# Kernel tuning notes

Hardware: AMD Instinct MI355X
Metric: run time of the kernel (lower is better)

The kernel has to match this reference:

```python
import jax, jax.numpy as jnp
import numpy as np

BS, GRID, LSTM_H, CNN_C, PROJ = 256, 49, 512, 2048, 512


def setup_inputs() -> dict:
    key = jax.random.key(0)
    ks = jax.random.split(key, 7)
    s = lambda fan_in: 1.0 / np.sqrt(fan_in)
    return {
        "lstm_hidden": jax.random.normal(ks[0], (BS, LSTM_H), jnp.float32),
        "cnn_feat": jax.random.normal(ks[1], (BS, GRID, CNN_C), jnp.float32),
        "W_lstm": jax.random.normal(ks[2], (PROJ, LSTM_H), jnp.float32) * s(LSTM_H),
        "b_lstm": jax.random.normal(ks[3], (PROJ,), jnp.float32) * s(LSTM_H),
        "W_cnn": jax.random.normal(ks[4], (PROJ, CNN_C), jnp.float32) * s(CNN_C),
        "b_cnn": jax.random.normal(ks[5], (PROJ,), jnp.float32) * s(CNN_C),
        "w_attn": jax.random.normal(ks[6], (1, PROJ), jnp.float32) * s(PROJ),
    }


def reference(lstm_hidden, cnn_feat, W_lstm, b_lstm, W_cnn, b_cnn, w_attn):
    # H computed once (original loop recomputes it per grid, identically)
    H = lstm_hidden @ W_lstm.T + b_lstm                       # (bs, P)
    V = jnp.einsum("bgc,pc->bgp", cnn_feat, W_cnn) + b_cnn    # (bs, G, P)
    z = jnp.tanh(H[:, None, :] + V) @ w_attn[0]               # (bs, G)
    bs, G = z.shape
    # Faithful to torch: cat over grids along dim 0 -> (G*bs,), then view(bs, G)
    z_scrambled = jnp.swapaxes(z, 0, 1).reshape(bs, G)
    return jax.nn.softmax(z_scrambled, axis=1)
```

## Files before the change

kernel.cpp:

```cpp
#include <hip/hip_runtime.h>
#include <math.h>

#define BSZ    256
#define GRID_N 49
#define LSTMH  512
#define CNN_C  2048
#define PROJ   512
#define KAUG   2560
#define M_TOT  12544
#define BK     64
#define KTILES (KAUG / BK)

#define MT2    128
#define NT2    128
#define NBLK2  ((M_TOT / MT2) * (PROJ / NT2))

#define MT     64
#define NT     128
#define NBLK   ((M_TOT / MT) * (PROJ / NT))

#define WBLK   640

typedef short bf16x8 __attribute__((ext_vector_type(8)));
typedef float f32x4  __attribute__((ext_vector_type(4)));

static __device__ __forceinline__ unsigned short bf16_rne(float f) {
    unsigned int u = __float_as_uint(f);
    u = u + 0x7FFFu + ((u >> 16) & 1u);
    return (unsigned short)(u >> 16);
}
static __device__ __forceinline__ uint4 pack8f(const float* f) {
    uint4 o;
    o.x = (unsigned int)bf16_rne(f[0]) | ((unsigned int)bf16_rne(f[1]) << 16);
    o.y = (unsigned int)bf16_rne(f[2]) | ((unsigned int)bf16_rne(f[3]) << 16);
    o.z = (unsigned int)bf16_rne(f[4]) | ((unsigned int)bf16_rne(f[5]) << 16);
    o.w = (unsigned int)bf16_rne(f[6]) | ((unsigned int)bf16_rne(f[7]) << 16);
    return o;
}
static __device__ __forceinline__ float tanh_fast(float x) {
    float e = __expf(2.f * x);
    return 1.f - 2.f / (e + 1.f);
}
static __device__ __forceinline__ void glds16(const void* g, void* l) {
    __builtin_amdgcn_global_load_lds(
        (const __attribute__((address_space(1))) unsigned int*)g,
        (__attribute__((address_space(3))) unsigned int*)l, 16, 0, 0);
}

__global__ __launch_bounds__(256) void prep_w(const float* __restrict__ Wc,
                                              const float* __restrict__ Wl,
                                              unsigned short* __restrict__ wsW,
                                              float* __restrict__ out) {
    const int bid = blockIdx.x, t = threadIdx.x;
    if (bid < 49) out[bid * 256 + t] = 0.f;
    int c  = bid * 256 + t;
    int p  = c / 320;
    int kc = (c % 320) * 8;
    const float* src = (kc < CNN_C) ? (Wc + (size_t)p * CNN_C + kc)
                                    : (Wl + (size_t)p * LSTMH + (kc - CNN_C));
    float f[8];
    *(float4*)&f[0] = ((const float4*)src)[0];
    *(float4*)&f[4] = ((const float4*)src)[1];
    *(uint4*)(wsW + (size_t)p * KAUG + kc) = pack8f(f);
}

__global__ __launch_bounds__(256, 2) void gemm3(
    const float* __restrict__ lstm, const float* __restrict__ cnn,
    const unsigned short* __restrict__ wsW,
    const float* __restrict__ bl, const float* __restrict__ bc,
    const float* __restrict__ wat, float* __restrict__ out)
{
    __shared__ unsigned short Ab[2][MT2][BK];
    __shared__ unsigned short Bb[2][NT2][BK];

    const int t   = threadIdx.x;
    const int w   = t >> 6;
    const int l   = t & 63;
    const int q   = l >> 4;
    const int r16 = l & 15;
    const int wr  = w >> 1;
    const int wc  = w & 1;

    const int bid = (int)blockIdx.x;
    const int swz = (bid & 7) * (NBLK2 / 8) + (bid >> 3);
    const int m0  = (swz >> 2) * MT2;
    const int n0  = (swz & 3) * NT2;

    const int ar  = t >> 1;
    const int ac0 = (t & 1) * 4;
    const int sw  = ar & 7;
    const int grow = m0 + ar;
    const int ab_  = grow / 49;
    const int ag_  = grow - ab_ * 49;
    const float* cnnb  = cnn + ((size_t)ab_ * GRID_N + ag_) * CNN_C;
    const float* lstmb = lstm + (size_t)ab_ * LSTMH;

    const int srow = l >> 3;
    const int cg   = (l & 7) ^ srow;

    float4 fa[8];
    auto a_load = [&](int k0) {
        const float* s = (((k0 < CNN_C) ? (cnnb + k0) : (lstmb + (k0 - CNN_C)))) + ac0 * 8;
        #pragma unroll
        for (int i = 0; i < 8; ++i) fa[i] = ((const float4*)s)[i];
    };
    auto a_write = [&](int bufi) {
        #pragma unroll
        for (int c = 0; c < 4; ++c) {
            float f[8];
            *(float4*)&f[0] = fa[2 * c];
            *(float4*)&f[4] = fa[2 * c + 1];
            *(uint4*)&Ab[bufi][ar][((ac0 + c) ^ sw) * 8] = pack8f(f);
        }
    };
    auto b_stage = [&](int k0, int bufi) {
        #pragma unroll
        for (int jj = 0; jj < 4; ++jj) {
            const int rowb = w * 32 + jj * 8;
            const unsigned short* g = wsW + (size_t)(n0 + rowb + srow) * KAUG + k0 + cg * 8;
            glds16(g, &Bb[bufi][rowb][0]);
        }
    };

    f32x4 acc[4][4];
    #pragma unroll
    for (int mt = 0; mt < 4; ++mt)
        #pragma unroll
        for (int nt = 0; nt < 4; ++nt)
            acc[mt][nt] = (f32x4){0.f, 0.f, 0.f, 0.f};

    a_load(0);
    a_write(0);
    b_stage(0, 0);
    asm volatile("s_waitcnt vmcnt(0) lgkmcnt(0)" ::: "memory");
    __builtin_amdgcn_s_barrier();

    int cur = 0;
    for (int kt = 0; kt < KTILES; ++kt) {
        const bool more = (kt + 1 < KTILES);
        if (more) {
            a_load((kt + 1) * BK);
            b_stage((kt + 1) * BK, cur ^ 1);
        }
        #pragma unroll
        for (int ks = 0; ks < 2; ++ks) {
            const int cp = ((ks * 4 + q) ^ (r16 & 7)) * 8;
            bf16x8 af[4], bfr[4];
            #pragma unroll
            for (int mt = 0; mt < 4; ++mt)
                af[mt] = *(const bf16x8*)&Ab[cur][wr * 64 + mt * 16 + r16][cp];
            #pragma unroll
            for (int nt = 0; nt < 4; ++nt)
                bfr[nt] = *(const bf16x8*)&Bb[cur][wc * 64 + nt * 16 + r16][cp];
            #pragma unroll
            for (int mt = 0; mt < 4; ++mt)
                #pragma unroll
                for (int nt = 0; nt < 4; ++nt)
                    acc[mt][nt] = __builtin_amdgcn_mfma_f32_16x16x32_bf16(
                        af[mt], bfr[nt], acc[mt][nt], 0, 0, 0);
        }
        if (more) a_write(cur ^ 1);
        asm volatile("s_waitcnt vmcnt(0) lgkmcnt(0)" ::: "memory");
        __builtin_amdgcn_s_barrier();
        cur ^= 1;
    }

    float* zpf = (float*)&Ab[0][0][0];
    float part[4][4];
    #pragma unroll
    for (int mt = 0; mt < 4; ++mt)
        #pragma unroll
        for (int rr = 0; rr < 4; ++rr) part[mt][rr] = 0.f;
    #pragma unroll
    for (int nt = 0; nt < 4; ++nt) {
        const int p = n0 + wc * 64 + nt * 16 + r16;
        const float bb = bl[p] + bc[p];
        const float wa = wat[p];
        #pragma unroll
        for (int mt = 0; mt < 4; ++mt)
            #pragma unroll
            for (int rr = 0; rr < 4; ++rr)
                part[mt][rr] += tanh_fast(acc[mt][nt][rr] + bb) * wa;
    }
    #pragma unroll
    for (int mt = 0; mt < 4; ++mt)
        #pragma unroll
        for (int rr = 0; rr < 4; ++rr) {
            float v = part[mt][rr];
            v += __shfl_xor(v, 1);
            v += __shfl_xor(v, 2);
            v += __shfl_xor(v, 4);
            v += __shfl_xor(v, 8);
            if (r16 == 0) zpf[wc * MT2 + wr * 64 + mt * 16 + q * 4 + rr] = v;
        }
    __syncthreads();
    if (t < MT2) {
        const float v = zpf[t] + zpf[MT2 + t];
        const int row = m0 + t;
        const int b2  = row / 49;
        const int g2  = row - b2 * 49;
        atomicAdd(&out[g2 * BSZ + b2], v);
    }
}

__global__ __launch_bounds__(256, 4) void gemm_k(
    const float* __restrict__ lstm, const float* __restrict__ cnn,
    const float* __restrict__ Wc,   const float* __restrict__ Wl,
    const float* __restrict__ bl,   const float* __restrict__ bc,
    const float* __restrict__ wat,  float* __restrict__ out)
{
    __shared__ unsigned short Ash[MT][BK];
    __shared__ unsigned short Bsh[NT][BK];
    __shared__ float zp[4][MT];

    const int t   = threadIdx.x;
    const int w   = t >> 6;
    const int l   = t & 63;
    const int q   = l >> 4;
    const int r16 = l & 15;

    const int bid = (int)blockIdx.x;
    const int swz = (bid & 7) * (NBLK / 8) + (bid >> 3);
    const int m0 = (swz >> 2) * MT;
    const int n0 = (swz & 3) * NT;

    const int ra  = t >> 2;
    const int ca0 = t & 3;
    const int sa  = ra & 7;
    const int grow = m0 + ra;
    const int ab   = grow / 49;
    const int ag   = grow - ab * 49;
    const float* cnnb  = cnn + ((size_t)ab * GRID_N + ag) * CNN_C;
    const float* lstmb = lstm + (size_t)ab * LSTMH;

    f32x4 acc[4][2];
    #pragma unroll
    for (int mt = 0; mt < 4; ++mt)
        #pragma unroll
        for (int nt = 0; nt < 2; ++nt)
            acc[mt][nt] = (f32x4){0.f, 0.f, 0.f, 0.f};

    float4 fa0, fa1, fa2, fa3;

    auto a_load = [&](int k0) {
        const float* s = (k0 < CNN_C) ? (cnnb + k0) : (lstmb + (k0 - CNN_C));
        const float4* p0 = (const float4*)(s + ca0 * 8);
        const float4* p1 = (const float4*)(s + (ca0 + 4) * 8);
        fa0 = p0[0]; fa1 = p0[1];
        fa2 = p1[0]; fa3 = p1[1];
    };
    auto a_write = [&]() {
        float f[8];
        *(float4*)&f[0] = fa0; *(float4*)&f[4] = fa1;
        *(uint4*)&Ash[ra][(ca0 ^ sa) * 8] = pack8f(f);
        *(float4*)&f[0] = fa2; *(float4*)&f[4] = fa3;
        *(uint4*)&Ash[ra][((ca0 + 4) ^ sa) * 8] = pack8f(f);
    };
    auto b_stage = [&](int k0) {
        const int rb = t >> 1;
        const int hb = t & 1;
        const float* s = (k0 < CNN_C) ? (Wc + (size_t)(n0 + rb) * CNN_C + k0)
                                      : (Wl + (size_t)(n0 + rb) * LSTMH + (k0 - CNN_C));
        const int sw = rb & 7;
        #pragma unroll
        for (int c = 0; c < 4; ++c) {
            const int cc = hb * 4 + c;
            float f[8];
            *(float4*)&f[0] = ((const float4*)(s + cc * 8))[0];
            *(float4*)&f[4] = ((const float4*)(s + cc * 8))[1];
            *(uint4*)&Bsh[rb][(cc ^ sw) * 8] = pack8f(f);
        }
    };

    a_load(0);
    a_write();
    b_stage(0);

    for (int kt = 0; kt < KTILES; ++kt) {
        __syncthreads();
        const bool more = (kt + 1 < KTILES);
        if (more) a_load((kt + 1) * BK);
        #pragma unroll
        for (int ks = 0; ks < 2; ++ks) {
            const int cp = ((ks * 4 + q) ^ (r16 & 7)) * 8;
            bf16x8 af[4], bfr[2];
            #pragma unroll
            for (int mt = 0; mt < 4; ++mt)
                af[mt] = *(const bf16x8*)&Ash[mt * 16 + r16][cp];
            #pragma unroll
            for (int nt = 0; nt < 2; ++nt)
                bfr[nt] = *(const bf16x8*)&Bsh[w * 32 + nt * 16 + r16][cp];
            #pragma unroll
            for (int mt = 0; mt < 4; ++mt)
                #pragma unroll
                for (int nt = 0; nt < 2; ++nt)
                    acc[mt][nt] = __builtin_amdgcn_mfma_f32_16x16x32_bf16(
                        af[mt], bfr[nt], acc[mt][nt], 0, 0, 0);
        }
        __syncthreads();
        if (more) { a_write(); b_stage((kt + 1) * BK); }
    }

    float part[4][4];
    #pragma unroll
    for (int mt = 0; mt < 4; ++mt)
        #pragma unroll
        for (int rr = 0; rr < 4; ++rr) part[mt][rr] = 0.f;
    #pragma unroll
    for (int nt = 0; nt < 2; ++nt) {
        const int p = n0 + w * 32 + nt * 16 + r16;
        const float bb = bl[p] + bc[p];
        const float wa = wat[p];
        #pragma unroll
        for (int mt = 0; mt < 4; ++mt)
            #pragma unroll
            for (int rr = 0; rr < 4; ++rr)
                part[mt][rr] += tanh_fast(acc[mt][nt][rr] + bb) * wa;
    }
    #pragma unroll
    for (int mt = 0; mt < 4; ++mt)
        #pragma unroll
        for (int rr = 0; rr < 4; ++rr) {
            float v = part[mt][rr];
            v += __shfl_xor(v, 1);
            v += __shfl_xor(v, 2);
            v += __shfl_xor(v, 4);
            v += __shfl_xor(v, 8);
            if (r16 == 0) zp[w][mt * 16 + q * 4 + rr] = v;
        }
    __syncthreads();
    if (t < MT) {
        const float v = zp[0][t] + zp[1][t] + zp[2][t] + zp[3][t];
        const int row = m0 + t;
        const int b2  = row / 49;
        const int g2  = row - b2 * 49;
        atomicAdd(&out[g2 * BSZ + b2], v);
    }
}

__global__ __launch_bounds__(64) void softmax_rows(float* __restrict__ out)
{
    const int i = blockIdx.x;
    const int j = threadIdx.x;
    float x = (j < GRID_N) ? out[i * GRID_N + j] : -1e30f;
    float m = x;
    #pragma unroll
    for (int off = 32; off > 0; off >>= 1) m = fmaxf(m, __shfl_xor(m, off));
    float e = (j < GRID_N) ? __expf(x - m) : 0.f;
    float s = e;
    #pragma unroll
    for (int off = 32; off > 0; off >>= 1) s += __shfl_xor(s, off);
    if (j < GRID_N) out[i * GRID_N + j] = e / s;
}

extern "C" void kernel_launch(void* const* d_in, const int* in_sizes, int n_in,
                              void* d_out, int out_size, void* d_ws, size_t ws_size,
                              hipStream_t stream)
{
    const float* lstm = (const float*)d_in[0];
    const float* cnn  = (const float*)d_in[1];
    const float* Wl   = (const float*)d_in[2];
    const float* bl   = (const float*)d_in[3];
    const float* Wc   = (const float*)d_in[4];
    const float* bc   = (const float*)d_in[5];
    const float* wat  = (const float*)d_in[6];
    float* out = (float*)d_out;

    const size_t szW = (size_t)PROJ * KAUG * sizeof(unsigned short);

    if (ws_size >= szW) {
        unsigned short* wsW = (unsigned short*)d_ws;
        prep_w<<<dim3(WBLK), dim3(256), 0, stream>>>(Wc, Wl, wsW, out);
        gemm3<<<dim3(NBLK2), dim3(256), 0, stream>>>(lstm, cnn, wsW, bl, bc, wat, out);
    } else {
        hipMemsetAsync(out, 0, (size_t)out_size * sizeof(float), stream);
        gemm_k<<<dim3(NBLK), dim3(256), 0, stream>>>(lstm, cnn, Wc, Wl, bl, bc, wat, out);
    }
    softmax_rows<<<dim3(BSZ), dim3(64), 0, stream>>>(out);
}
```

Before: 265.0 us.

## Deepen GEMM prefetch pipeline to two tiles ahead with partial vmcnt waits

Reworks the main GEMM loop so A global loads and B global-to-LDS copies are issued two K-tiles ahead, with partial vmcnt waits instead of draining all outstanding memory ops every iteration. The A tile for the next step is packed and written to LDS before the MFMA block, and the B copy for tile kt+2 is issued after the compute barrier. The fp32-to-bf16 packing also switches to the hardware v_cvt_pk_bf16_f32 instruction. This is meant to hide global memory latency behind the MFMAs, at the cost of more registers held in flight and a fragile hand-counted vmcnt value.

```diff
diff --git a/kernel.cpp b/kernel.cpp
--- a/kernel.cpp
+++ b/kernel.cpp
@@ -64,7 +64,7 @@
     *(uint4*)(wsW + (size_t)p * KAUG + kc) = pack8f(f);
 }
 
-__global__ __launch_bounds__(256, 2) void gemm3(
+__global__ __launch_bounds__(256, 2) void gemm9(
     const float* __restrict__ lstm, const float* __restrict__ cnn,
     const unsigned short* __restrict__ wsW,
     const float* __restrict__ bl, const float* __restrict__ bc,
@@ -85,6 +85,9 @@
     const int swz = (bid & 7) * (NBLK2 / 8) + (bid >> 3);
     const int m0  = (swz >> 2) * MT2;
     const int n0  = (swz & 3) * NT2;
+
+    const int srow = l >> 3;
+    const int cg   = (l & 7) ^ srow;
 
     const int ar  = t >> 1;
     const int ac0 = (t & 1) * 4;
@@ -95,28 +98,30 @@
     const float* cnnb  = cnn + ((size_t)ab_ * GRID_N + ag_) * CNN_C;
     const float* lstmb = lstm + (size_t)ab_ * LSTMH;
 
-    const int srow = l >> 3;
-    const int cg   = (l & 7) ^ srow;
-
     float4 fa[8];
-    auto a_load = [&](int k0) {
+    auto a_load = [&](int kt) {
+        const int k0 = kt * BK;
         const float* s = (((k0 < CNN_C) ? (cnnb + k0) : (lstmb + (k0 - CNN_C)))) + ac0 * 8;
         #pragma unroll
         for (int i = 0; i < 8; ++i) fa[i] = ((const float4*)s)[i];
     };
-    auto a_write = [&](int bufi) {
+    auto a_pack_write = [&](int bufi) {
         #pragma unroll
         for (int c = 0; c < 4; ++c) {
-            float f[8];
-            *(float4*)&f[0] = fa[2 * c];
-            *(float4*)&f[4] = fa[2 * c + 1];
-            *(uint4*)&Ab[bufi][ar][((ac0 + c) ^ sw) * 8] = pack8f(f);
-        }
-    };
-    auto b_stage = [&](int k0, int bufi) {
-        #pragma unroll
-        for (int jj = 0; jj < 4; ++jj) {
-            const int rowb = w * 32 + jj * 8;
+            const float4 x = fa[2 * c], y = fa[2 * c + 1];
+            uint4 o;
+            asm("v_cvt_pk_bf16_f32 %0, %1, %2" : "=v"(o.x) : "v"(x.x), "v"(x.y));
+            asm("v_cvt_pk_bf16_f32 %0, %1, %2" : "=v"(o.y) : "v"(x.z), "v"(x.w));
+            asm("v_cvt_pk_bf16_f32 %0, %1, %2" : "=v"(o.z) : "v"(y.x), "v"(y.y));
+            asm("v_cvt_pk_bf16_f32 %0, %1, %2" : "=v"(o.w) : "v"(y.z), "v"(y.w));
+            *(uint4*)&Ab[bufi][ar][((ac0 + c) ^ sw) * 8] = o;
+        }
+    };
+    auto b_stage = [&](int kt, int bufi) {
+        const int k0 = kt * BK;
+        #pragma unroll
+        for (int j = 0; j < 4; ++j) {
+            const int rowb = w * 32 + j * 8;
             const unsigned short* g = wsW + (size_t)(n0 + rowb + srow) * KAUG + k0 + cg * 8;
             glds16(g, &Bb[bufi][rowb][0]);
         }
@@ -130,18 +135,23 @@
             acc[mt][nt] = (f32x4){0.f, 0.f, 0.f, 0.f};
 
     a_load(0);
-    a_write(0);
     b_stage(0, 0);
-    asm volatile("s_waitcnt vmcnt(0) lgkmcnt(0)" ::: "memory");
-    __builtin_amdgcn_s_barrier();
-
-    int cur = 0;
+    a_pack_write(0);
+    a_load(1);
+    b_stage(1, 1);
+    asm volatile("s_waitcnt lgkmcnt(0)" ::: "memory");
+
     for (int kt = 0; kt < KTILES; ++kt) {
-        const bool more = (kt + 1 < KTILES);
-        if (more) {
-            a_load((kt + 1) * BK);
-            b_stage((kt + 1) * BK, cur ^ 1);
-        }
+        const int cur = kt & 1;
+        if (kt + 1 < KTILES) {
+            asm volatile("s_waitcnt vmcnt(12)" ::: "memory");
+        } else {
+            asm volatile("s_waitcnt vmcnt(0)" ::: "memory");
+        }
+        __builtin_amdgcn_s_barrier();
+        if (kt + 1 < KTILES) a_pack_write(cur ^ 1);
+        if (kt + 2 < KTILES) a_load(kt + 2);
+        __builtin_amdgcn_sched_barrier(0);
         #pragma unroll
         for (int ks = 0; ks < 2; ++ks) {
             const int cp = ((ks * 4 + q) ^ (r16 & 7)) * 8;
@@ -159,10 +169,9 @@
                     acc[mt][nt] = __builtin_amdgcn_mfma_f32_16x16x32_bf16(
                         af[mt], bfr[nt], acc[mt][nt], 0, 0, 0);
         }
-        if (more) a_write(cur ^ 1);
-        asm volatile("s_waitcnt vmcnt(0) lgkmcnt(0)" ::: "memory");
+        asm volatile("s_waitcnt lgkmcnt(0)" ::: "memory");
         __builtin_amdgcn_s_barrier();
-        cur ^= 1;
+        if (kt + 2 < KTILES) b_stage(kt + 2, cur);
     }
 
     float* zpf = (float*)&Ab[0][0][0];
@@ -371,7 +380,7 @@
     if (ws_size >= szW) {
         unsigned short* wsW = (unsigned short*)d_ws;
         prep_w<<<dim3(WBLK), dim3(256), 0, stream>>>(Wc, Wl, wsW, out);
-        gemm3<<<dim3(NBLK2), dim3(256), 0, stream>>>(lstm, cnn, wsW, bl, bc, wat, out);
+        gemm9<<<dim3(NBLK2), dim3(256), 0, stream>>>(lstm, cnn, wsW, bl, bc, wat, out);
     } else {
         hipMemsetAsync(out, 0, (size_t)out_size * sizeof(float), stream);
         gemm_k<<<dim3(NBLK), dim3(256), 0, stream>>>(lstm, cnn, Wc, Wl, bl, bc, wat, out);
```

Result: faster. 253.7 us (-4.3%).
